# Performance work log

Hardware: AMD Instinct MI355X
Metric: run time of the kernel (lower is better)

The kernel has to match this reference:

```python
import jax, jax.numpy as jnp
import numpy as np

I1, I2, N = 256, 256, 512
B = 2048
FLAT = (I1 + 1) * (I2 + 1)  # 66049


def setup_inputs() -> dict:
    key = jax.random.key(0)
    k1, k2, k3, k4 = jax.random.split(key, 4)
    s1 = 1.0 / np.sqrt(FLAT)
    s2 = 1.0 / np.sqrt(N)
    return {
        "inp1": jax.random.normal(k1, (B, I1), dtype=jnp.float32),
        "inp2": jax.random.normal(k2, (B, I2), dtype=jnp.float32),
        "W1": jax.random.normal(k3, (FLAT, N), dtype=jnp.float32) * s1,
        "b1": jnp.zeros((N,), dtype=jnp.float32),
        "W2": jax.random.normal(k4, (N, N), dtype=jnp.float32) * s2,
        "b2": jnp.zeros((N,), dtype=jnp.float32),
    }


def reference(inp1, inp2, W1, b1, W2, b2):
    b = inp1.shape[0]
    ones = jnp.ones((b, 1), dtype=inp1.dtype)
    a = jnp.concatenate([inp1, ones], axis=-1)  # [B, I1+1]
    c = jnp.concatenate([inp2, ones], axis=-1)  # [B, I2+1]
    # per-sample outer product, flattened: [B, (I1+1)*(I2+1)]
    fusion = jnp.einsum("bi,bj->bij", a, c).reshape(b, -1)
    h = jax.nn.relu(fusion @ W1 + b1)
    return jax.nn.relu(h @ W2 + b2)
```

## Files before the change

kernel.cpp:

```cpp
#include <hip/hip_runtime.h>
#include <hip/hip_bf16.h>
#include <stdint.h>

#define BATCH 2048
#define NHID  512
#define KMAIN 65792
#define KPAD  66112
#define NSTEP_ALL 1033
#define AW 320
#define CW 256

typedef __attribute__((ext_vector_type(8))) short short8;
typedef __attribute__((ext_vector_type(4))) short short4v;
typedef __attribute__((ext_vector_type(4))) float f32x4;

#define AS1 __attribute__((address_space(1)))
#define AS3 __attribute__((address_space(3)))

__device__ __forceinline__ unsigned short f2bf(float f) {
    union { float f; unsigned int u; } v; v.f = f;
    unsigned int r = v.u + 0x7FFFu + ((v.u >> 16) & 1u);
    return (unsigned short)(r >> 16);
}
__device__ __forceinline__ float bf2f(unsigned short u) {
    union { unsigned int i; float f; } v; v.i = ((unsigned int)u) << 16;
    return v.f;
}
__device__ __forceinline__ f32x4 MFMA16(short8 a, short8 b, f32x4 c) {
    return __builtin_amdgcn_mfma_f32_16x16x32_bf16(a, b, c, 0, 0, 0);
}

__device__ __forceinline__ int w1_src_row(int k) {
    if (k < KMAIN) return (k >> 8) * 257 + (k & 255);
    int i = k - KMAIN;
    return (i < 257) ? (i * 257 + 256) : -1;
}

__global__ __launch_bounds__(256) void prep_kernel(
        const float* __restrict__ inp1, const float* __restrict__ inp2,
        const float* __restrict__ W1, const float* __restrict__ W2,
        unsigned short* __restrict__ W1f, unsigned short* __restrict__ W2t,
        unsigned short* __restrict__ a_tab, unsigned short* __restrict__ c_tab) {
    __shared__ float T[64][65];
    int b = blockIdx.x;
    int t = threadIdx.x;

    if (b < 8264) {
        int kt = b % 1033, nt = b / 1033;
        int k0 = kt * 64, n0 = nt * 64;
        int nn = t & 63, kk0 = t >> 6;
#pragma unroll
        for (int it = 0; it < 16; ++it) {
            int kk = it * 4 + kk0;
            int row = w1_src_row(k0 + kk);
            T[kk][nn] = (row >= 0) ? W1[(long)row * NHID + n0 + nn] : 0.f;
        }
        __syncthreads();
#pragma unroll
        for (int it = 0; it < 2; ++it) {
            int id = it * 256 + t;
            int n16l = id >> 7;
            int kk   = (id >> 6) & 1;
            int lw   = id & 63;
            short8 o;
#pragma unroll
            for (int e = 0; e < 8; ++e)
                o[e] = (short)f2bf(T[kk * 32 + (lw >> 4) * 8 + e][n16l * 16 + (lw & 15)]);
            size_t off = ((size_t)(((n0 >> 4) + n16l) * NSTEP_ALL + kt) * 2 + kk) * 512
                         + (size_t)lw * 8;
            *reinterpret_cast<short8*>(&W1f[off]) = o;
        }
    } else if (b < 8264 + 64) {
        int bb = b - 8264;
        int kt = bb & 7, nt = bb >> 3;
        int k0 = kt * 64, n0 = nt * 64;
        int nn = t & 63, kk0 = t >> 6;
#pragma unroll
        for (int it = 0; it < 16; ++it) {
            int kk = it * 4 + kk0;
            T[kk][nn] = W2[(long)(k0 + kk) * NHID + n0 + nn];
        }
        __syncthreads();
#pragma unroll
        for (int it = 0; it < 2; ++it) {
            int idx = it * 256 + t;
            int nl = idx >> 3, ch = idx & 7;
            short8 o;
#pragma unroll
            for (int e = 0; e < 8; ++e) o[e] = (short)f2bf(T[ch * 8 + e][nl]);
            *reinterpret_cast<short8*>(&W2t[(long)(n0 + nl) * NHID + k0 + ch * 8]) = o;
        }
    } else {
        int r0 = (b - 8328) * 32;
        for (int idx = t; idx < 32 * (AW / 8); idx += 256) {
            int r = idx / 40, ch = idx - r * 40;
            int m = r0 + r;
            short8 o;
#pragma unroll
            for (int e = 0; e < 8; ++e) {
                int i = ch * 8 + e;
                float v = (i < 256) ? inp1[m * 256 + i] : (i == 256 ? 1.0f : 0.0f);
                o[e] = (short)f2bf(v);
            }
            *reinterpret_cast<short8*>(&a_tab[m * AW + ch * 8]) = o;
        }
        for (int idx = t; idx < 32 * (CW / 8); idx += 256) {
            int r = idx >> 5, ch = idx & 31;
            int m = r0 + r;
            short8 o;
#pragma unroll
            for (int e = 0; e < 8; ++e) o[e] = (short)f2bf(inp2[m * 256 + ch * 8 + e]);
            *reinterpret_cast<short8*>(&c_tab[m * CW + ch * 8]) = o;
        }
    }
}

__device__ __forceinline__ void stage_tile128(const unsigned short* __restrict__ g,
        long row0, long k0, long ld, unsigned short* lds) {
    int t = threadIdx.x;
    int wave = t >> 6, lane = t & 63;
    int rl = lane >> 3;
    int ch = (lane & 7) ^ rl;
    const unsigned short* src0 = g + (row0 + wave * 8 + rl) * ld + k0 + ch * 8;
#pragma unroll
    for (int r = 0; r < 4; ++r) {
        const unsigned short* src = src0 + (long)r * 32 * ld;
        unsigned short* dst = lds + (r * 32 + wave * 8) * 64;
        __builtin_amdgcn_global_load_lds((const AS1 unsigned int*)src,
                                         (AS3 unsigned int*)dst, 16, 0, 0);
    }
}
__device__ __forceinline__ short8 read_frag(const unsigned short* lds,
        int rowbase, int kofs, int lane) {
    int row = rowbase + (lane & 15);
    int chunkL = (kofs >> 3) + (lane >> 4);
    int sw = chunkL ^ (row & 7);
    return *reinterpret_cast<const short8*>(&lds[row * 64 + sw * 8]);
}

__global__ __launch_bounds__(256, 2) void gemm1_kernel(
        const unsigned short* __restrict__ a_tab,
        const unsigned short* __restrict__ c_tab,
        const unsigned short* __restrict__ W1f, float* __restrict__ hacc) {
    __shared__ __align__(16) unsigned short a_win[65 * 256];

    int mb = blockIdx.x >> 6;
    int g8 = blockIdx.x & 63;
    int nt = g8 & 15;
    int s  = g8 >> 4;
    int st0 = s * 256;
    int ngroups = (s == 3) ? 65 : 64;

    int lane = threadIdx.x & 63;
    int wv   = threadIdx.x >> 6;
    int rowbase = mb * 256 + wv * 64;
    int frow = lane & 15;
    int kq = (lane >> 4) * 8;
    int r4 = (lane >> 4) * 4;
    int n16a = nt * 2, n16b = nt * 2 + 1;

    short8 cc[4][8];
#pragma unroll
    for (int fm = 0; fm < 4; ++fm)
#pragma unroll
        for (int q = 0; q < 8; ++q)
            cc[fm][q] = *reinterpret_cast<const short8*>(
                &c_tab[(size_t)(rowbase + fm * 16 + frow) * CW + kq + q * 32]);

    {
        const unsigned short* src = a_tab + (size_t)(mb * 256 + threadIdx.x) * AW + s * 64;
        for (int i = 0; i < 65; ++i) a_win[i * 256 + threadIdx.x] = src[i];
    }
    __syncthreads();

    f32x4 acc[4][2];
#pragma unroll
    for (int a = 0; a < 4; ++a)
#pragma unroll
        for (int b2 = 0; b2 < 2; ++b2) acc[a][b2] = (f32x4){0.f, 0.f, 0.f, 0.f};

    short8 bufE0, bufE1, bufE2, bufE3, bufO0, bufO1, bufO2, bufO3;

#define LOADSTEP(st, D) do { \
    const unsigned short* _p0 = W1f + ((size_t)(n16a * NSTEP_ALL + (st))) * 1024 + lane * 8; \
    const unsigned short* _p1 = W1f + ((size_t)(n16b * NSTEP_ALL + (st))) * 1024 + lane * 8; \
    D##0 = *reinterpret_cast<const short8*>(_p0); \
    D##1 = *reinterpret_cast<const short8*>(_p0 + 512); \
    D##2 = *reinterpret_cast<const short8*>(_p1); \
    D##3 = *reinterpret_cast<const short8*>(_p1 + 512); \
} while (0)
#define MFSTEP(B, p) do { \
    _Pragma("unroll") \
    for (int fm = 0; fm < 4; ++fm) { \
        P[fm][0] = MFMA16(cc[fm][2 * (p)],     B##0, P[fm][0]); \
        P[fm][1] = MFMA16(cc[fm][2 * (p)],     B##2, P[fm][1]); \
        P[fm][0] = MFMA16(cc[fm][2 * (p) + 1], B##1, P[fm][0]); \
        P[fm][1] = MFMA16(cc[fm][2 * (p) + 1], B##3, P[fm][1]); \
    } \
} while (0)

    LOADSTEP(st0, bufE);

    for (int g = 0; g < ngroups; ++g) {
        int stg = st0 + g * 4;
        f32x4 P[4][2];
#pragma unroll
        for (int a = 0; a < 4; ++a)
#pragma unroll
            for (int b2 = 0; b2 < 2; ++b2) P[a][b2] = (f32x4){0.f, 0.f, 0.f, 0.f};

        LOADSTEP(stg + 1, bufO);  MFSTEP(bufE, 0);
        LOADSTEP(stg + 2, bufE);  MFSTEP(bufO, 1);
        LOADSTEP(stg + 3, bufO);  MFSTEP(bufE, 2);
        LOADSTEP(stg + 4, bufE);  MFSTEP(bufO, 3);

#pragma unroll
        for (int fm = 0; fm < 4; ++fm) {
            short4v a4 = *reinterpret_cast<const short4v*>(
                &a_win[g * 256 + wv * 64 + fm * 16 + r4]);
#pragma unroll
            for (int r = 0; r < 4; ++r) {
                float av = bf2f((unsigned short)a4[r]);
                acc[fm][0][r] += av * P[fm][0][r];
                acc[fm][1][r] += av * P[fm][1][r];
            }
        }
    }

    if (s == 3) {
#define TAILMF(B, p) do { \
    _Pragma("unroll") \
    for (int fm = 0; fm < 4; ++fm) { \
        const unsigned short* _ar = a_tab + (size_t)(rowbase + fm * 16 + frow) * AW + (p) * 64 + kq; \
        short8 t0 = *reinterpret_cast<const short8*>(_ar); \
        short8 t1 = *reinterpret_cast<const short8*>(_ar + 32); \
        acc[fm][0] = MFMA16(t0, B##0, acc[fm][0]); \
        acc[fm][1] = MFMA16(t0, B##2, acc[fm][1]); \
        acc[fm][0] = MFMA16(t1, B##1, acc[fm][0]); \
        acc[fm][1] = MFMA16(t1, B##3, acc[fm][1]); \
    } \
} while (0)
        LOADSTEP(1029, bufO);  TAILMF(bufE, 0);
        LOADSTEP(1030, bufE);  TAILMF(bufO, 1);
        LOADSTEP(1031, bufO);  TAILMF(bufE, 2);
        LOADSTEP(1032, bufE);  TAILMF(bufO, 3);
        TAILMF(bufE, 4);
    }

#pragma unroll
    for (int fm = 0; fm < 4; ++fm)
#pragma unroll
        for (int fn = 0; fn < 2; ++fn)
#pragma unroll
            for (int r = 0; r < 4; ++r) {
                int row = rowbase + fm * 16 + r4 + r;
                int col = nt * 32 + fn * 16 + frow;
                atomicAdd(&hacc[row * NHID + col], acc[fm][fn][r]);
            }
}

__global__ __launch_bounds__(256) void bias_relu_h_kernel(
        const float* __restrict__ hacc, const float* __restrict__ b1,
        unsigned short* __restrict__ h) {
    int idx = blockIdx.x * 256 + threadIdx.x;
    f32x4 v = ((const f32x4*)hacc)[idx];
    int col = (idx & 127) << 2;
    f32x4 bb = *(const f32x4*)(b1 + col);
    short4v o;
#pragma unroll
    for (int e = 0; e < 4; ++e) {
        float x = v[e] + bb[e];
        x = fmaxf(x, 0.f);
        o[e] = (short)f2bf(x);
    }
    ((short4v*)h)[idx] = o;
}

__global__ __launch_bounds__(256) void gemm2_kernel(
        const unsigned short* __restrict__ h, const unsigned short* __restrict__ W2t,
        const float* __restrict__ b2, float* __restrict__ out) {
    __shared__ unsigned short A_s[128 * 64];
    __shared__ unsigned short B_s[128 * 64];
    int m0 = (blockIdx.x >> 2) * 128;
    int n0 = (blockIdx.x & 3) * 128;
    int lane = threadIdx.x & 63;
    int wv = threadIdx.x >> 6;
    int wm = (wv >> 1) * 64;
    int wn = (wv & 1) * 64;

    f32x4 acc[4][4];
#pragma unroll
    for (int a = 0; a < 4; ++a)
#pragma unroll
        for (int b = 0; b < 4; ++b) acc[a][b] = (f32x4){0.f, 0.f, 0.f, 0.f};

    for (int st = 0; st < 8; ++st) {
        int kbase = st * 64;
        __syncthreads();
        stage_tile128(h,   m0, kbase, NHID, A_s);
        stage_tile128(W2t, n0, kbase, NHID, B_s);
        __syncthreads();
#pragma unroll
        for (int kk = 0; kk < 2; ++kk) {
            short8 aF[4], bF[4];
#pragma unroll
            for (int fm = 0; fm < 4; ++fm) aF[fm] = read_frag(A_s, wm + fm * 16, kk * 32, lane);
#pragma unroll
            for (int fn = 0; fn < 4; ++fn) bF[fn] = read_frag(B_s, wn + fn * 16, kk * 32, lane);
#pragma unroll
            for (int fm = 0; fm < 4; ++fm)
#pragma unroll
                for (int fn = 0; fn < 4; ++fn)
                    acc[fm][fn] = __builtin_amdgcn_mfma_f32_16x16x32_bf16(
                        aF[fm], bF[fn], acc[fm][fn], 0, 0, 0);
        }
    }
    int cl = lane & 15;
    int r4 = (lane >> 4) * 4;
#pragma unroll
    for (int fm = 0; fm < 4; ++fm)
#pragma unroll
        for (int fn = 0; fn < 4; ++fn)
#pragma unroll
            for (int r = 0; r < 4; ++r) {
                int row = m0 + wm + fm * 16 + r4 + r;
                int col = n0 + wn + fn * 16 + cl;
                float x = acc[fm][fn][r] + b2[col];
                out[row * NHID + col] = fmaxf(x, 0.f);
            }
}

extern "C" void kernel_launch(void* const* d_in, const int* in_sizes, int n_in,
                              void* d_out, int out_size, void* d_ws, size_t ws_size,
                              hipStream_t stream) {
    const float* inp1 = (const float*)d_in[0];
    const float* inp2 = (const float*)d_in[1];
    const float* W1   = (const float*)d_in[2];
    const float* b1   = (const float*)d_in[3];
    const float* W2   = (const float*)d_in[4];
    const float* b2   = (const float*)d_in[5];
    float* out = (float*)d_out;

    size_t off = 0;
    auto alloc = [&](size_t bytes) {
        void* p = (char*)d_ws + off;
        off += (bytes + 255) & ~(size_t)255;
        return p;
    };
    unsigned short* W1f   = (unsigned short*)alloc((size_t)32 * NSTEP_ALL * 1024 * 2);
    unsigned short* W2t   = (unsigned short*)alloc((size_t)NHID * NHID * 2);
    unsigned short* h     = (unsigned short*)alloc((size_t)BATCH * NHID * 2);
    unsigned short* a_tab = (unsigned short*)alloc((size_t)BATCH * AW * 2);
    unsigned short* c_tab = (unsigned short*)alloc((size_t)BATCH * CW * 2);
    (void)ws_size; (void)in_sizes; (void)n_in; (void)out_size;

    hipMemsetAsync(d_out, 0, (size_t)BATCH * NHID * 4, stream);

    prep_kernel<<<8264 + 64 + 64, 256, 0, stream>>>(inp1, inp2, W1, W2,
                                                    W1f, W2t, a_tab, c_tab);

    gemm1_kernel<<<512, 256, 0, stream>>>(a_tab, c_tab, W1f, (float*)d_out);
    bias_relu_h_kernel<<<(BATCH * NHID / 4) / 256, 256, 0, stream>>>((const float*)d_out, b1, h);
    gemm2_kernel<<<64, 256, 0, stream>>>(h, W2t, b2, out);
}
```

Baseline: 182.0 us.

## Split GEMM1 K into six slices and fuse bias-ReLU into GEMM2 staging

GEMM1 is regridded from four to six K-slices per tile (768 blocks) with a smaller LDS window and a launch bound allowing three blocks per CU, to raise occupancy and latency hiding. The separate bias+ReLU+bf16 conversion kernel is removed; GEMM2 now reads the fp32 accumulator directly and applies bias/ReLU while staging into LDS. This adds more atomic traffic and register pressure in GEMM1, and GEMM2 staging becomes synchronous loads instead of direct-to-LDS copies.

Measured after the change: 466.8 us. 156% more time.

```diff
diff --git a/kernel.cpp b/kernel.cpp
--- a/kernel.cpp
+++ b/kernel.cpp
@@ -5,10 +5,10 @@
 #define BATCH 2048
 #define NHID  512
 #define KMAIN 65792
-#define KPAD  66112
 #define NSTEP_ALL 1033
 #define AW 320
 #define CW 256
+#define IPS 43
 
 typedef __attribute__((ext_vector_type(8))) short short8;
 typedef __attribute__((ext_vector_type(4))) short short4v;
@@ -130,6 +130,29 @@
                                          (AS3 unsigned int*)dst, 16, 0, 0);
     }
 }
+__device__ __forceinline__ void stage_h_tile(const float* __restrict__ hacc,
+        const float* __restrict__ b1, int row0, int k0, unsigned short* lds) {
+    int t = threadIdx.x;
+    int wave = t >> 6, lane = t & 63;
+    int rl = lane >> 3;
+    int ch = lane & 7;
+    int swch = ch ^ rl;
+    f32x4 b0 = *(const f32x4*)(b1 + k0 + ch * 8);
+    f32x4 b4 = *(const f32x4*)(b1 + k0 + ch * 8 + 4);
+#pragma unroll
+    for (int r = 0; r < 4; ++r) {
+        int row = r * 32 + wave * 8 + rl;
+        const float* src = hacc + (size_t)(row0 + row) * NHID + k0 + ch * 8;
+        f32x4 v0 = *(const f32x4*)src;
+        f32x4 v4 = *(const f32x4*)(src + 4);
+        short8 o;
+#pragma unroll
+        for (int e = 0; e < 4; ++e) o[e]     = (short)f2bf(fmaxf(v0[e] + b0[e], 0.f));
+#pragma unroll
+        for (int e = 0; e < 4; ++e) o[4 + e] = (short)f2bf(fmaxf(v4[e] + b4[e], 0.f));
+        *reinterpret_cast<short8*>(&lds[row * 64 + swch * 8]) = o;
+    }
+}
 __device__ __forceinline__ short8 read_frag(const unsigned short* lds,
         int rowbase, int kofs, int lane) {
     int row = rowbase + (lane & 15);
@@ -138,18 +161,19 @@
     return *reinterpret_cast<const short8*>(&lds[row * 64 + sw * 8]);
 }
 
-__global__ __launch_bounds__(256, 2) void gemm1_kernel(
+__global__ __launch_bounds__(256, 3) void gemm1_kernel(
         const unsigned short* __restrict__ a_tab,
         const unsigned short* __restrict__ c_tab,
         const unsigned short* __restrict__ W1f, float* __restrict__ hacc) {
-    __shared__ __align__(16) unsigned short a_win[65 * 256];
-
-    int mb = blockIdx.x >> 6;
-    int g8 = blockIdx.x & 63;
-    int nt = g8 & 15;
-    int s  = g8 >> 4;
-    int st0 = s * 256;
-    int ngroups = (s == 3) ? 65 : 64;
+    __shared__ __align__(16) unsigned short a_win[IPS * 256];
+
+    int mb = blockIdx.x / 96;
+    int g96 = blockIdx.x % 96;
+    int nt = g96 / 6;
+    int s  = g96 % 6;
+    int i0 = s * IPS;
+    int ngroups = (s == 5) ? 42 : IPS;
+    int st0 = i0 * 4;
 
     int lane = threadIdx.x & 63;
     int wv   = threadIdx.x >> 6;
@@ -168,8 +192,8 @@
                 &c_tab[(size_t)(rowbase + fm * 16 + frow) * CW + kq + q * 32]);
 
     {
-        const unsigned short* src = a_tab + (size_t)(mb * 256 + threadIdx.x) * AW + s * 64;
-        for (int i = 0; i < 65; ++i) a_win[i * 256 + threadIdx.x] = src[i];
+        const unsigned short* src = a_tab + (size_t)(mb * 256 + threadIdx.x) * AW + i0;
+        for (int i = 0; i < ngroups; ++i) a_win[i * 256 + threadIdx.x] = src[i];
     }
     __syncthreads();
 
@@ -227,7 +251,7 @@
         }
     }
 
-    if (s == 3) {
+    if (s == 5) {
 #define TAILMF(B, p) do { \
     _Pragma("unroll") \
     for (int fm = 0; fm < 4; ++fm) { \
@@ -259,25 +283,9 @@
             }
 }
 
-__global__ __launch_bounds__(256) void bias_relu_h_kernel(
+__global__ __launch_bounds__(256) void gemm2_kernel(
         const float* __restrict__ hacc, const float* __restrict__ b1,
-        unsigned short* __restrict__ h) {
-    int idx = blockIdx.x * 256 + threadIdx.x;
-    f32x4 v = ((const f32x4*)hacc)[idx];
-    int col = (idx & 127) << 2;
-    f32x4 bb = *(const f32x4*)(b1 + col);
-    short4v o;
-#pragma unroll
-    for (int e = 0; e < 4; ++e) {
-        float x = v[e] + bb[e];
-        x = fmaxf(x, 0.f);
-        o[e] = (short)f2bf(x);
-    }
-    ((short4v*)h)[idx] = o;
-}
-
-__global__ __launch_bounds__(256) void gemm2_kernel(
-        const unsigned short* __restrict__ h, const unsigned short* __restrict__ W2t,
+        const unsigned short* __restrict__ W2t,
         const float* __restrict__ b2, float* __restrict__ out) {
     __shared__ unsigned short A_s[128 * 64];
     __shared__ unsigned short B_s[128 * 64];
@@ -297,8 +305,8 @@
     for (int st = 0; st < 8; ++st) {
         int kbase = st * 64;
         __syncthreads();
-        stage_tile128(h,   m0, kbase, NHID, A_s);
         stage_tile128(W2t, n0, kbase, NHID, B_s);
+        stage_h_tile(hacc, b1, m0, kbase, A_s);
         __syncthreads();
 #pragma unroll
         for (int kk = 0; kk < 2; ++kk) {
@@ -349,17 +357,16 @@
     };
     unsigned short* W1f   = (unsigned short*)alloc((size_t)32 * NSTEP_ALL * 1024 * 2);
     unsigned short* W2t   = (unsigned short*)alloc((size_t)NHID * NHID * 2);
-    unsigned short* h     = (unsigned short*)alloc((size_t)BATCH * NHID * 2);
+    float*          hacc  = (float*)alloc((size_t)BATCH * NHID * 4);
     unsigned short* a_tab = (unsigned short*)alloc((size_t)BATCH * AW * 2);
     unsigned short* c_tab = (unsigned short*)alloc((size_t)BATCH * CW * 2);
     (void)ws_size; (void)in_sizes; (void)n_in; (void)out_size;
 
-    hipMemsetAsync(d_out, 0, (size_t)BATCH * NHID * 4, stream);
+    hipMemsetAsync(hacc, 0, (size_t)BATCH * NHID * 4, stream);
 
     prep_kernel<<<8264 + 64 + 64, 256, 0, stream>>>(inp1, inp2, W1, W2,
                                                     W1f, W2t, a_tab, c_tab);
 
-    gemm1_kernel<<<512, 256, 0, stream>>>(a_tab, c_tab, W1f, (float*)d_out);
-    bias_relu_h_kernel<<<(BATCH * NHID / 4) / 256, 256, 0, stream>>>((const float*)d_out, b1, h);
-    gemm2_kernel<<<64, 256, 0, stream>>>(h, W2t, b2, out);
-}
+    gemm1_kernel<<<768, 256, 0, stream>>>(a_tab, c_tab, W1f, hacc);
+    gemm2_kernel<<<64, 256, 0, stream>>>(hacc, b1, W2t, b2, out);
+}
```
